# Optimization experiments

Hardware: AMD Instinct MI355X
Metric: run time of the kernel (lower is better)

## Reference

```python
import jax, jax.numpy as jnp
import numpy as np

B, T, D, H = 4, 2048, 1024, 16
HS = D // H  # 64
EPS = 1e-5


def layer_norm(x, g, b):
    mu = jnp.mean(x, axis=-1, keepdims=True)
    var = jnp.mean(jnp.square(x - mu), axis=-1, keepdims=True)
    return (x - mu) * jax.lax.rsqrt(var + EPS) * g + b


def setup_inputs() -> dict:
    key = jax.random.key(0)
    ks = jax.random.split(key, 12)
    s_in = 1.0 / np.sqrt(D)
    s_proj = 1.0 / np.sqrt(H * HS)
    s_ff = 1.0 / np.sqrt(4 * D)
    return {
        "x": jax.random.normal(ks[0], (B, T, D), jnp.float32),
        "ln1_g": jnp.ones((D,), jnp.float32),
        "ln1_b": jnp.zeros((D,), jnp.float32),
        # per-head Q/K/V weights stacked: [H, D, HS] (x @ W, no bias)
        "wq": jax.random.uniform(ks[1], (H, D, HS), jnp.float32, -s_in, s_in),
        "wk": jax.random.uniform(ks[2], (H, D, HS), jnp.float32, -s_in, s_in),
        "wv": jax.random.uniform(ks[3], (H, D, HS), jnp.float32, -s_in, s_in),
        "w_proj": jax.random.uniform(ks[4], (H * HS, D), jnp.float32, -s_proj, s_proj),
        "b_proj": jax.random.uniform(ks[5], (D,), jnp.float32, -s_proj, s_proj),
        "ln2_g": jnp.ones((D,), jnp.float32),
        "ln2_b": jnp.zeros((D,), jnp.float32),
        "w1": jax.random.uniform(ks[6], (D, 4 * D), jnp.float32, -s_in, s_in),
        "b1": jax.random.uniform(ks[7], (4 * D,), jnp.float32, -s_in, s_in),
        "w2": jax.random.uniform(ks[8], (4 * D, D), jnp.float32, -s_ff, s_ff),
        "b2": jax.random.uniform(ks[9], (D,), jnp.float32, -s_ff, s_ff),
    }


def reference(x, ln1_g, ln1_b, wq, wk, wv, w_proj, b_proj, ln2_g, ln2_b, w1, b1, w2, b2):
    # --- pre-LN self-attention ---
    xn = layer_norm(x, ln1_g, ln1_b)
    q = jnp.einsum("btd,hdk->bhtk", xn, wq)
    k = jnp.einsum("btd,hdk->bhtk", xn, wk)
    v = jnp.einsum("btd,hdk->bhtk", xn, wv)
    scale = HS ** -0.5
    scores = jnp.einsum("bhtk,bhsk->bhts", q, k) * scale  # [B,H,T,T]
    t = x.shape[1]
    causal = jnp.tril(jnp.ones((t, t), bool))
    scores = jnp.where(causal, scores, -jnp.inf)
    attn = jax.nn.softmax(scores, axis=-1)  # dropout p=0 -> identity
    ctx = jnp.einsum("bhts,bhsk->bhtk", attn, v)
    ctx = jnp.transpose(ctx, (0, 2, 1, 3)).reshape(x.shape[0], t, H * HS)
    x = x + ctx @ w_proj + b_proj
    # --- pre-LN feed-forward ---
    xn = layer_norm(x, ln2_g, ln2_b)
    h = jax.nn.relu(xn @ w1 + b1)
    return x + h @ w2 + b2
```

## Files before the change

### kernel.cpp

```cpp
#include <hip/hip_runtime.h>

typedef __bf16 bf16;
typedef __attribute__((ext_vector_type(8))) __bf16 bf16x8;
typedef __attribute__((ext_vector_type(4))) __bf16 bf16x4;
typedef __attribute__((ext_vector_type(4))) float f32x4;

static constexpr int Bc = 4, Tc = 2048, Dc = 1024, Hc = 16, HSc = 64, DFF = 4096;
static constexpr int Mrows = Bc * Tc;

#define DEV __device__ __forceinline__

DEV void load_lds16(const void* g, void* l) {
  __builtin_amdgcn_global_load_lds(
      (const __attribute__((address_space(1))) void*)g,
      (__attribute__((address_space(3))) void*)l, 16, 0, 0);
}

__global__ void repack_qkv_kernel(const float* __restrict__ wq,
                                  const float* __restrict__ wk,
                                  const float* __restrict__ wv,
                                  bf16* __restrict__ dst) {
  __shared__ float tile[64][65];
  const int dblk = blockIdx.x;
  const int z = blockIdx.y;
  const int w = z >> 4, h = z & 15;
  const float* src = (w == 0 ? wq : (w == 1 ? wk : wv)) + (size_t)h * Dc * HSc;
  const int tx = threadIdx.x, ty = threadIdx.y;
#pragma unroll
  for (int i = 0; i < 16; ++i)
    tile[ty + i * 4][tx] = src[(size_t)(dblk * 64 + ty + i * 4) * HSc + tx];
  __syncthreads();
#pragma unroll
  for (int i = 0; i < 16; ++i) {
    const int s = ty + i * 4;
    dst[((size_t)w * 1024 + h * 64 + s) * Dc + dblk * 64 + tx] = (bf16)tile[tx][s];
  }
}

__global__ void transpose_to_bf16_kernel(const float* __restrict__ src,
                                         bf16* __restrict__ dst, int R, int C) {
  __shared__ float tile[64][65];
  const int r0 = blockIdx.x * 64, c0 = blockIdx.y * 64;
  const int tx = threadIdx.x, ty = threadIdx.y;
#pragma unroll
  for (int i = 0; i < 16; ++i)
    tile[ty + i * 4][tx] = src[(size_t)(r0 + ty + i * 4) * C + c0 + tx];
  __syncthreads();
#pragma unroll
  for (int i = 0; i < 16; ++i)
    dst[(size_t)(c0 + ty + i * 4) * R + r0 + tx] = (bf16)tile[tx][ty + i * 4];
}

__global__ __launch_bounds__(256) void ln_kernel(const float* __restrict__ x,
                                                 const float* __restrict__ gam,
                                                 const float* __restrict__ bet,
                                                 bf16* __restrict__ out) {
  const int row = blockIdx.x;
  const int t = threadIdx.x;
  const float4 v = ((const float4*)(x + (size_t)row * Dc))[t];
  float s = v.x + v.y + v.z + v.w;
  float s2 = v.x * v.x + v.y * v.y + v.z * v.z + v.w * v.w;
#pragma unroll
  for (int m = 1; m < 64; m <<= 1) {
    s += __shfl_xor(s, m);
    s2 += __shfl_xor(s2, m);
  }
  __shared__ float red[8];
  const int wid = t >> 6;
  if ((t & 63) == 0) { red[wid * 2] = s; red[wid * 2 + 1] = s2; }
  __syncthreads();
  s = red[0] + red[2] + red[4] + red[6];
  s2 = red[1] + red[3] + red[5] + red[7];
  const float mean = s * (1.f / Dc);
  const float var = s2 * (1.f / Dc) - mean * mean;
  const float rstd = rsqrtf(var + 1e-5f);
  const float4 gv = ((const float4*)gam)[t];
  const float4 bv = ((const float4*)bet)[t];
  bf16x4 o;
  o[0] = (bf16)((v.x - mean) * rstd * gv.x + bv.x);
  o[1] = (bf16)((v.y - mean) * rstd * gv.y + bv.y);
  o[2] = (bf16)((v.z - mean) * rstd * gv.z + bv.z);
  o[3] = (bf16)((v.w - mean) * rstd * gv.w + bv.w);
  *(bf16x4*)(out + (size_t)row * Dc + t * 4) = o;
}

template <int MODE, int KTOT, int NSTRIDE>
__global__ __launch_bounds__(256, 2) void gemm_kernel(
    const bf16* __restrict__ A, const bf16* __restrict__ BT,
    const float* __restrict__ bias, const float* __restrict__ resid,
    float* __restrict__ outf, bf16* __restrict__ outb,
    bf16* __restrict__ qo, bf16* __restrict__ ko, bf16* __restrict__ vto) {
  __shared__ __attribute__((aligned(16))) bf16 As[128 * 32];
  __shared__ __attribute__((aligned(16))) bf16 Bs[128 * 32];
  const int tid = threadIdx.x;
  const int wid = tid >> 6, lane = tid & 63;
  const int g = lane >> 4, c = lane & 15;
  const int wr = wid >> 1, wc = wid & 1;
  const int bm = blockIdx.x, bn = blockIdx.y;

  f32x4 acc[4][4];
#pragma unroll
  for (int i = 0; i < 4; ++i)
#pragma unroll
    for (int j = 0; j < 4; ++j)
#pragma unroll
      for (int r = 0; r < 4; ++r) acc[i][j][r] = 0.f;

  const bf16* gA = A + (size_t)(bm * 128 + wid * 32 + (lane >> 2)) * KTOT + (lane & 3) * 8;
  const bf16* gB = BT + (size_t)(bn * 128 + wid * 32 + (lane >> 2)) * KTOT + (lane & 3) * 8;
  bf16* lA0 = &As[(wid * 32) * 32];
  bf16* lA1 = &As[(wid * 32 + 16) * 32];
  bf16* lB0 = &Bs[(wid * 32) * 32];
  bf16* lB1 = &Bs[(wid * 32 + 16) * 32];

  for (int kt = 0; kt < KTOT / 32; ++kt) {
    load_lds16(gA, lA0);
    load_lds16(gA + (size_t)16 * KTOT, lA1);
    load_lds16(gB, lB0);
    load_lds16(gB + (size_t)16 * KTOT, lB1);
    gA += 32;
    gB += 32;
    __syncthreads();
    bf16x8 af[4], bfr[4];
#pragma unroll
    for (int mi = 0; mi < 4; ++mi)
      af[mi] = *(const bf16x8*)&As[(wr * 64 + mi * 16 + c) * 32 + g * 8];
#pragma unroll
    for (int ni = 0; ni < 4; ++ni)
      bfr[ni] = *(const bf16x8*)&Bs[(wc * 64 + ni * 16 + c) * 32 + g * 8];
#pragma unroll
    for (int mi = 0; mi < 4; ++mi)
#pragma unroll
      for (int ni = 0; ni < 4; ++ni)
        acc[mi][ni] =
            __builtin_amdgcn_mfma_f32_16x16x32_bf16(af[mi], bfr[ni], acc[mi][ni], 0, 0, 0);
    __syncthreads();
  }

#pragma unroll
  for (int ni = 0; ni < 4; ++ni) {
    const int n = bn * 128 + wc * 64 + ni * 16 + c;
    float bi = 0.f;
    if (MODE != 0) bi = bias[n];
#pragma unroll
    for (int mi = 0; mi < 4; ++mi) {
      const int m0 = bm * 128 + wr * 64 + mi * 16 + g * 4;
      if (MODE == 0) {
        const int w = n >> 10, n1 = n & 1023, h = n1 >> 6, sidx = n1 & 63;
        const int b = m0 >> 11, t0 = m0 & 2047;
        if (w == 0) {
#pragma unroll
          for (int r = 0; r < 4; ++r)
            qo[(size_t)(b * Hc + h) * (Tc * HSc) + (size_t)(t0 + r) * HSc + sidx] =
                (bf16)(acc[mi][ni][r] * 0.125f);
        } else if (w == 1) {
#pragma unroll
          for (int r = 0; r < 4; ++r)
            ko[(size_t)(b * Hc + h) * (Tc * HSc) + (size_t)(t0 + r) * HSc + sidx] =
                (bf16)acc[mi][ni][r];
        } else {
          bf16x4 pk;
#pragma unroll
          for (int r = 0; r < 4; ++r) pk[r] = (bf16)acc[mi][ni][r];
          *(bf16x4*)&vto[((size_t)(b * Hc + h) * HSc + sidx) * Tc + t0] = pk;
        }
      } else if (MODE == 1 || MODE == 3) {
#pragma unroll
        for (int r = 0; r < 4; ++r) {
          const size_t idx = (size_t)(m0 + r) * NSTRIDE + n;
          outf[idx] = acc[mi][ni][r] + bi + resid[idx];
        }
      } else {
#pragma unroll
        for (int r = 0; r < 4; ++r)
          outb[(size_t)(m0 + r) * NSTRIDE + n] = (bf16)fmaxf(acc[mi][ni][r] + bi, 0.f);
      }
    }
  }
}

__global__ __launch_bounds__(64, 2) void attn_kernel(const bf16* __restrict__ q,
                                                     const bf16* __restrict__ k,
                                                     const bf16* __restrict__ vt,
                                                     bf16* __restrict__ ctx) {
  __shared__ __attribute__((aligned(16))) bf16 P[32][72];
  const int d0 = blockIdx.x;
  const int L = (d0 & 7) * 256 + (d0 >> 3);
  const int bh = L >> 5, w = L & 31;
  const int lane = threadIdx.x;
  const int g = lane >> 4, c = lane & 15;
  const bf16* qh = q + (size_t)bh * Tc * HSc;
  const bf16* kh = k + (size_t)bh * Tc * HSc;
  const bf16* vh = vt + (size_t)bh * HSc * Tc;
  const int b = bh >> 4, h = bh & 15;

  for (int half = 0; half < 2; ++half) {
    const int qt = half ? w : 63 - w;
    const int ktmax = (qt * 32 + 31) >> 6;
    const bf16* qb = qh + (size_t)qt * 32 * HSc;

    bf16x8 qf[2][2];
#pragma unroll
    for (int mi = 0; mi < 2; ++mi)
#pragma unroll
      for (int kk = 0; kk < 2; ++kk)
        qf[mi][kk] = *(const bf16x8*)&qb[(size_t)(mi * 16 + c) * HSc + kk * 32 + g * 8];

    f32x4 o[2][4];
    float m_[2][4], ls[2][4];
#pragma unroll
    for (int mi = 0; mi < 2; ++mi)
#pragma unroll
      for (int r = 0; r < 4; ++r) {
        m_[mi][r] = -1e30f;
        ls[mi][r] = 0.f;
#pragma unroll
        for (int di = 0; di < 4; ++di) o[mi][di][r] = 0.f;
      }

    auto loadK = [&](bf16x8 (&kf)[4][2], int kt) {
      const bf16* kb = kh + (size_t)kt * 64 * HSc;
#pragma unroll
      for (int ni = 0; ni < 4; ++ni)
#pragma unroll
        for (int kk = 0; kk < 2; ++kk)
          kf[ni][kk] = *(const bf16x8*)&kb[(size_t)(ni * 16 + c) * HSc + kk * 32 + g * 8];
    };

    auto body = [&](bf16x8 (&kf)[4][2], int kt) {
      const bf16* vb = vh + kt * 64;
      bf16x8 vf[4][2];
#pragma unroll
      for (int di = 0; di < 4; ++di)
#pragma unroll
        for (int kk = 0; kk < 2; ++kk)
          vf[di][kk] = *(const bf16x8*)&vb[(size_t)(di * 16 + c) * Tc + kk * 32 + g * 8];

      f32x4 s[2][4];
#pragma unroll
      for (int mi = 0; mi < 2; ++mi)
#pragma unroll
        for (int ni = 0; ni < 4; ++ni)
#pragma unroll
          for (int r = 0; r < 4; ++r) s[mi][ni][r] = 0.f;
      __builtin_amdgcn_s_setprio(1);
#pragma unroll
      for (int kk = 0; kk < 2; ++kk)
#pragma unroll
        for (int mi = 0; mi < 2; ++mi)
#pragma unroll
          for (int ni = 0; ni < 4; ++ni)
            s[mi][ni] = __builtin_amdgcn_mfma_f32_16x16x32_bf16(qf[mi][kk], kf[ni][kk],
                                                                s[mi][ni], 0, 0, 0);
      __builtin_amdgcn_s_setprio(0);

      if (kt == ktmax) {
#pragma unroll
        for (int mi = 0; mi < 2; ++mi)
#pragma unroll
          for (int ni = 0; ni < 4; ++ni)
#pragma unroll
            for (int r = 0; r < 4; ++r) {
              const int row = qt * 32 + mi * 16 + g * 4 + r;
              const int col = kt * 64 + ni * 16 + c;
              if (col > row) s[mi][ni][r] = -1e30f;
            }
      }

      float pm[2][4];
      int need = 0;
#pragma unroll
      for (int mi = 0; mi < 2; ++mi)
#pragma unroll
        for (int r = 0; r < 4; ++r) {
          pm[mi][r] = fmaxf(fmaxf(s[mi][0][r], s[mi][1][r]), fmaxf(s[mi][2][r], s[mi][3][r]));
          need |= (pm[mi][r] > m_[mi][r] + 8.f) ? 1 : 0;
        }
      if (__any(need)) {
#pragma unroll
        for (int mi = 0; mi < 2; ++mi)
#pragma unroll
          for (int r = 0; r < 4; ++r) {
            float mx = pm[mi][r];
#pragma unroll
            for (int msk = 1; msk < 16; msk <<= 1) mx = fmaxf(mx, __shfl_xor(mx, msk));
            const float mn = fmaxf(m_[mi][r], mx);
            const float al = __expf(m_[mi][r] - mn);
            m_[mi][r] = mn;
            ls[mi][r] *= al;
#pragma unroll
            for (int di = 0; di < 4; ++di) o[mi][di][r] *= al;
          }
      }
#pragma unroll
      for (int mi = 0; mi < 2; ++mi)
#pragma unroll
        for (int r = 0; r < 4; ++r) {
          float ps = 0.f;
#pragma unroll
          for (int ni = 0; ni < 4; ++ni) {
            const float p = __expf(s[mi][ni][r] - m_[mi][r]);
            ps += p;
            P[mi * 16 + g * 4 + r][ni * 16 + c] = (bf16)p;
          }
          ls[mi][r] += ps;
        }
      asm volatile("s_waitcnt lgkmcnt(0)" ::: "memory");
      __builtin_amdgcn_sched_barrier(0);

      bf16x8 pf[2][2];
#pragma unroll
      for (int mi = 0; mi < 2; ++mi)
#pragma unroll
        for (int kk = 0; kk < 2; ++kk)
          pf[mi][kk] = *(const bf16x8*)&P[mi * 16 + c][kk * 32 + g * 8];
      __builtin_amdgcn_s_setprio(1);
#pragma unroll
      for (int kk = 0; kk < 2; ++kk)
#pragma unroll
        for (int mi = 0; mi < 2; ++mi)
#pragma unroll
          for (int di = 0; di < 4; ++di)
            o[mi][di] = __builtin_amdgcn_mfma_f32_16x16x32_bf16(pf[mi][kk], vf[di][kk],
                                                                o[mi][di], 0, 0, 0);
      __builtin_amdgcn_s_setprio(0);
    };

    bf16x8 kfA[4][2], kfB[4][2];
    loadK(kfA, 0);
    int kt = 0;
    while (true) {
      if (kt < ktmax) loadK(kfB, kt + 1);
      body(kfA, kt);
      if (kt >= ktmax) break;
      ++kt;
      if (kt < ktmax) loadK(kfA, kt + 1);
      body(kfB, kt);
      if (kt >= ktmax) break;
      ++kt;
    }

#pragma unroll
    for (int mi = 0; mi < 2; ++mi)
#pragma unroll
      for (int r = 0; r < 4; ++r) {
        float l = ls[mi][r];
#pragma unroll
        for (int msk = 1; msk < 16; msk <<= 1) l += __shfl_xor(l, msk);
        const float inv = 1.f / l;
        const int t = qt * 32 + mi * 16 + g * 4 + r;
#pragma unroll
        for (int di = 0; di < 4; ++di)
          ctx[((size_t)(b * Tc + t)) * Dc + h * 64 + di * 16 + c] =
              (bf16)(o[mi][di][r] * inv);
      }
  }
}

extern "C" void kernel_launch(void* const* d_in, const int* in_sizes, int n_in,
                              void* d_out, int out_size, void* d_ws, size_t ws_size,
                              hipStream_t stream) {
  (void)in_sizes; (void)n_in; (void)out_size; (void)ws_size;
  const float* x      = (const float*)d_in[0];
  const float* ln1_g  = (const float*)d_in[1];
  const float* ln1_b  = (const float*)d_in[2];
  const float* wq     = (const float*)d_in[3];
  const float* wk     = (const float*)d_in[4];
  const float* wv     = (const float*)d_in[5];
  const float* w_proj = (const float*)d_in[6];
  const float* b_proj = (const float*)d_in[7];
  const float* ln2_g  = (const float*)d_in[8];
  const float* ln2_b  = (const float*)d_in[9];
  const float* w1     = (const float*)d_in[10];
  const float* b1     = (const float*)d_in[11];
  const float* w2     = (const float*)d_in[12];
  const float* b2     = (const float*)d_in[13];
  float* out = (float*)d_out;
  char* ws = (char*)d_ws;

  bf16* qbuf   = (bf16*)(ws + 0);
  bf16* kbuf   = (bf16*)(ws + 16777216);
  bf16* vtbuf  = (bf16*)(ws + 33554432);
  bf16* ctxbuf = (bf16*)(ws + 50331648);
  bf16* wqkvT  = (bf16*)(ws + 67108864);
  bf16* hbuf   = (bf16*)(ws + 0);
  bf16* wprojT = (bf16*)(ws + 73400320);
  bf16* w1T    = (bf16*)(ws + 75497472);
  bf16* w2T    = (bf16*)(ws + 83886080);
  bf16* xn     = (bf16*)(ws + 92274688);
  float* x1buf = (float*)(ws + 109051904);

  repack_qkv_kernel<<<dim3(16, 48), dim3(64, 4), 0, stream>>>(wq, wk, wv, wqkvT);
  transpose_to_bf16_kernel<<<dim3(16, 16), dim3(64, 4), 0, stream>>>(w_proj, wprojT, 1024, 1024);
  transpose_to_bf16_kernel<<<dim3(16, 64), dim3(64, 4), 0, stream>>>(w1, w1T, 1024, 4096);
  transpose_to_bf16_kernel<<<dim3(64, 16), dim3(64, 4), 0, stream>>>(w2, w2T, 4096, 1024);

  ln_kernel<<<Mrows, 256, 0, stream>>>(x, ln1_g, ln1_b, xn);
  gemm_kernel<0, 1024, 0><<<dim3(64, 24), 256, 0, stream>>>(
      xn, wqkvT, nullptr, nullptr, nullptr, nullptr, qbuf, kbuf, vtbuf);
  attn_kernel<<<2048, 64, 0, stream>>>(qbuf, kbuf, vtbuf, ctxbuf);
  gemm_kernel<1, 1024, 1024><<<dim3(64, 8), 256, 0, stream>>>(
      ctxbuf, wprojT, b_proj, x, x1buf, nullptr, nullptr, nullptr, nullptr);
  ln_kernel<<<Mrows, 256, 0, stream>>>(x1buf, ln2_g, ln2_b, xn);
  gemm_kernel<2, 1024, 4096><<<dim3(64, 32), 256, 0, stream>>>(
      xn, w1T, b1, nullptr, nullptr, hbuf, nullptr, nullptr, nullptr);
  gemm_kernel<3, 4096, 1024><<<dim3(64, 8), 256, 0, stream>>>(
      hbuf, w2T, b2, x1buf, out, nullptr, nullptr, nullptr, nullptr);
}
```

Baseline: 457.5 us.

## Share K/V tiles across four waves via double-buffered swizzled LDS in attention

The attention kernel moves from single-wave blocks handling 32 query rows to 256-thread blocks where four waves cover 128 consecutive query rows. K and V tiles are staged once per block into double-buffered LDS using direct global-to-LDS loads with an XOR swizzle, so each wave reads them from LDS instead of loading its own copy from global memory. This is meant to cut redundant K/V global traffic and overlap loading with compute. In exchange it adds block-wide barriers each iteration and load imbalance, since waves with fewer causal tiles sit idle while the block stages tiles up to the last wave's limit.

Measured after the change: 392.2 us. -14.3%, faster.

```diff
diff --git a/kernel.cpp b/kernel.cpp
--- a/kernel.cpp
+++ b/kernel.cpp
@@ -179,25 +179,36 @@
   }
 }
 
-__global__ __launch_bounds__(64, 2) void attn_kernel(const bf16* __restrict__ q,
-                                                     const bf16* __restrict__ k,
-                                                     const bf16* __restrict__ vt,
-                                                     bf16* __restrict__ ctx) {
-  __shared__ __attribute__((aligned(16))) bf16 P[32][72];
+__global__ __launch_bounds__(256, 2) void attn_kernel(const bf16* __restrict__ q,
+                                                      const bf16* __restrict__ k,
+                                                      const bf16* __restrict__ vt,
+                                                      bf16* __restrict__ ctx) {
+  __shared__ __attribute__((aligned(16))) bf16 Kl[2][4096];
+  __shared__ __attribute__((aligned(16))) bf16 Vl[2][4096];
+  __shared__ __attribute__((aligned(16))) bf16 P[4][32][72];
   const int d0 = blockIdx.x;
-  const int L = (d0 & 7) * 256 + (d0 >> 3);
-  const int bh = L >> 5, w = L & 31;
-  const int lane = threadIdx.x;
+  const int L = (d0 & 7) * 64 + (d0 >> 3);
+  const int bh = L >> 3, p = L & 7;
+  const int tid = threadIdx.x;
+  const int wid = tid >> 6, lane = tid & 63;
   const int g = lane >> 4, c = lane & 15;
   const bf16* qh = q + (size_t)bh * Tc * HSc;
-  const bf16* kh = k + (size_t)bh * Tc * HSc;
-  const bf16* vh = vt + (size_t)bh * HSc * Tc;
+  const char* kh = (const char*)(k + (size_t)bh * Tc * HSc);
+  const char* vh = (const char*)(vt + (size_t)bh * HSc * Tc);
   const int b = bh >> 4, h = bh & 15;
 
-  for (int half = 0; half < 2; ++half) {
-    const int qt = half ? w : 63 - w;
-    const int ktmax = (qt * 32 + 31) >> 6;
-    const bf16* qb = qh + (size_t)qt * 32 * HSc;
+  const int sw = ((lane >> 3) & 7) << 4;
+  const int soK = (lane * 16) ^ sw;
+  const int vrow = lane >> 3;
+  const int vcol = ((lane & 7) * 16) ^ sw;
+  const int rsw = (c & 7) << 4;
+
+  for (int g2 = 0; g2 < 2; ++g2) {
+    const int grp = g2 ? p : 15 - p;
+    const int ktB = 2 * grp + 1;
+    const int ktW = 2 * grp + (wid >> 1);
+    const int row0 = grp * 128 + wid * 32;
+    const bf16* qb = qh + (size_t)row0 * HSc;
 
     bf16x8 qf[2][2];
 #pragma unroll
@@ -218,126 +229,132 @@
         for (int di = 0; di < 4; ++di) o[mi][di][r] = 0.f;
       }
 
-    auto loadK = [&](bf16x8 (&kf)[4][2], int kt) {
-      const bf16* kb = kh + (size_t)kt * 64 * HSc;
-#pragma unroll
-      for (int ni = 0; ni < 4; ++ni)
+    auto stage = [&](int buf, int kt) {
+      const char* kb = kh + (size_t)kt * 8192;
+      const char* vb = vh + (size_t)kt * 128;
+#pragma unroll
+      for (int i = 0; i < 4; ++i) {
+        const int idx = wid * 4 + i;
+        if (idx < 8) {
+          load_lds16(kb + idx * 1024 + soK, (char*)&Kl[buf][0] + idx * 1024);
+        } else {
+          const int j = idx - 8;
+          load_lds16(vb + (size_t)(j * 8 + vrow) * (Tc * 2) + vcol,
+                     (char*)&Vl[buf][0] + j * 1024);
+        }
+      }
+    };
+
+    stage(0, 0);
+    __syncthreads();
+    int cur = 0;
+    for (int kt = 0; kt <= ktB; ++kt) {
+      if (kt < ktB) stage(cur ^ 1, kt + 1);
+      if (kt <= ktW) {
+        const char* Kb = (const char*)&Kl[cur][0];
+        bf16x8 kf[4][2];
+#pragma unroll
+        for (int ni = 0; ni < 4; ++ni)
+#pragma unroll
+          for (int kk = 0; kk < 2; ++kk)
+            kf[ni][kk] = *(const bf16x8*)(Kb + (ni * 16 + c) * 128 +
+                                          (((kk << 6) | (g << 4)) ^ rsw));
+        f32x4 s[2][4];
+#pragma unroll
+        for (int mi = 0; mi < 2; ++mi)
+#pragma unroll
+          for (int ni = 0; ni < 4; ++ni)
+#pragma unroll
+            for (int r = 0; r < 4; ++r) s[mi][ni][r] = 0.f;
+        __builtin_amdgcn_s_setprio(1);
 #pragma unroll
         for (int kk = 0; kk < 2; ++kk)
-          kf[ni][kk] = *(const bf16x8*)&kb[(size_t)(ni * 16 + c) * HSc + kk * 32 + g * 8];
-    };
-
-    auto body = [&](bf16x8 (&kf)[4][2], int kt) {
-      const bf16* vb = vh + kt * 64;
-      bf16x8 vf[4][2];
-#pragma unroll
-      for (int di = 0; di < 4; ++di)
-#pragma unroll
-        for (int kk = 0; kk < 2; ++kk)
-          vf[di][kk] = *(const bf16x8*)&vb[(size_t)(di * 16 + c) * Tc + kk * 32 + g * 8];
-
-      f32x4 s[2][4];
-#pragma unroll
-      for (int mi = 0; mi < 2; ++mi)
-#pragma unroll
-        for (int ni = 0; ni < 4; ++ni)
-#pragma unroll
-          for (int r = 0; r < 4; ++r) s[mi][ni][r] = 0.f;
-      __builtin_amdgcn_s_setprio(1);
-#pragma unroll
-      for (int kk = 0; kk < 2; ++kk)
+#pragma unroll
+          for (int mi = 0; mi < 2; ++mi)
+#pragma unroll
+            for (int ni = 0; ni < 4; ++ni)
+              s[mi][ni] = __builtin_amdgcn_mfma_f32_16x16x32_bf16(qf[mi][kk], kf[ni][kk],
+                                                                  s[mi][ni], 0, 0, 0);
+        __builtin_amdgcn_s_setprio(0);
+
+        if (kt == ktW) {
+#pragma unroll
+          for (int mi = 0; mi < 2; ++mi)
+#pragma unroll
+            for (int ni = 0; ni < 4; ++ni)
+#pragma unroll
+              for (int r = 0; r < 4; ++r) {
+                const int row = row0 + mi * 16 + g * 4 + r;
+                const int col = kt * 64 + ni * 16 + c;
+                if (col > row) s[mi][ni][r] = -1e30f;
+              }
+        }
+
+        float pm[2][4];
+        int need = 0;
 #pragma unroll
         for (int mi = 0; mi < 2; ++mi)
 #pragma unroll
-          for (int ni = 0; ni < 4; ++ni)
-            s[mi][ni] = __builtin_amdgcn_mfma_f32_16x16x32_bf16(qf[mi][kk], kf[ni][kk],
-                                                                s[mi][ni], 0, 0, 0);
-      __builtin_amdgcn_s_setprio(0);
-
-      if (kt == ktmax) {
+          for (int r = 0; r < 4; ++r) {
+            pm[mi][r] =
+                fmaxf(fmaxf(s[mi][0][r], s[mi][1][r]), fmaxf(s[mi][2][r], s[mi][3][r]));
+            need |= (pm[mi][r] > m_[mi][r] + 8.f) ? 1 : 0;
+          }
+        if (__any(need)) {
+#pragma unroll
+          for (int mi = 0; mi < 2; ++mi)
+#pragma unroll
+            for (int r = 0; r < 4; ++r) {
+              float mx = pm[mi][r];
+#pragma unroll
+              for (int msk = 1; msk < 16; msk <<= 1) mx = fmaxf(mx, __shfl_xor(mx, msk));
+              const float mn = fmaxf(m_[mi][r], mx);
+              const float al = __expf(m_[mi][r] - mn);
+              m_[mi][r] = mn;
+              ls[mi][r] *= al;
+#pragma unroll
+              for (int di = 0; di < 4; ++di) o[mi][di][r] *= al;
+            }
+        }
 #pragma unroll
         for (int mi = 0; mi < 2; ++mi)
 #pragma unroll
-          for (int ni = 0; ni < 4; ++ni)
-#pragma unroll
-            for (int r = 0; r < 4; ++r) {
-              const int row = qt * 32 + mi * 16 + g * 4 + r;
-              const int col = kt * 64 + ni * 16 + c;
-              if (col > row) s[mi][ni][r] = -1e30f;
+          for (int r = 0; r < 4; ++r) {
+            float ps = 0.f;
+#pragma unroll
+            for (int ni = 0; ni < 4; ++ni) {
+              const float pv = __expf(s[mi][ni][r] - m_[mi][r]);
+              ps += pv;
+              P[wid][mi * 16 + g * 4 + r][ni * 16 + c] = (bf16)pv;
             }
+            ls[mi][r] += ps;
+          }
+        asm volatile("s_waitcnt lgkmcnt(0)" ::: "memory");
+        __builtin_amdgcn_sched_barrier(0);
+
+        bf16x8 pf[2][2];
+#pragma unroll
+        for (int mi = 0; mi < 2; ++mi)
+#pragma unroll
+          for (int kk = 0; kk < 2; ++kk)
+            pf[mi][kk] = *(const bf16x8*)&P[wid][mi * 16 + c][kk * 32 + g * 8];
+        const char* Vb = (const char*)&Vl[cur][0];
+#pragma unroll
+        for (int di = 0; di < 4; ++di) {
+          bf16x8 vf0 = *(const bf16x8*)(Vb + (di * 16 + c) * 128 + ((g << 4) ^ rsw));
+          bf16x8 vf1 =
+              *(const bf16x8*)(Vb + (di * 16 + c) * 128 + (((1 << 6) | (g << 4)) ^ rsw));
+          __builtin_amdgcn_s_setprio(1);
+#pragma unroll
+          for (int mi = 0; mi < 2; ++mi) {
+            o[mi][di] = __builtin_amdgcn_mfma_f32_16x16x32_bf16(pf[mi][0], vf0, o[mi][di], 0, 0, 0);
+            o[mi][di] = __builtin_amdgcn_mfma_f32_16x16x32_bf16(pf[mi][1], vf1, o[mi][di], 0, 0, 0);
+          }
+          __builtin_amdgcn_s_setprio(0);
+        }
       }
-
-      float pm[2][4];
-      int need = 0;
-#pragma unroll
-      for (int mi = 0; mi < 2; ++mi)
-#pragma unroll
-        for (int r = 0; r < 4; ++r) {
-          pm[mi][r] = fmaxf(fmaxf(s[mi][0][r], s[mi][1][r]), fmaxf(s[mi][2][r], s[mi][3][r]));
-          need |= (pm[mi][r] > m_[mi][r] + 8.f) ? 1 : 0;
-        }
-      if (__any(need)) {
-#pragma unroll
-        for (int mi = 0; mi < 2; ++mi)
-#pragma unroll
-          for (int r = 0; r < 4; ++r) {
-            float mx = pm[mi][r];
-#pragma unroll
-            for (int msk = 1; msk < 16; msk <<= 1) mx = fmaxf(mx, __shfl_xor(mx, msk));
-            const float mn = fmaxf(m_[mi][r], mx);
-            const float al = __expf(m_[mi][r] - mn);
-            m_[mi][r] = mn;
-            ls[mi][r] *= al;
-#pragma unroll
-            for (int di = 0; di < 4; ++di) o[mi][di][r] *= al;
-          }
-      }
-#pragma unroll
-      for (int mi = 0; mi < 2; ++mi)
-#pragma unroll
-        for (int r = 0; r < 4; ++r) {
-          float ps = 0.f;
-#pragma unroll
-          for (int ni = 0; ni < 4; ++ni) {
-            const float p = __expf(s[mi][ni][r] - m_[mi][r]);
-            ps += p;
-            P[mi * 16 + g * 4 + r][ni * 16 + c] = (bf16)p;
-          }
-          ls[mi][r] += ps;
-        }
-      asm volatile("s_waitcnt lgkmcnt(0)" ::: "memory");
-      __builtin_amdgcn_sched_barrier(0);
-
-      bf16x8 pf[2][2];
-#pragma unroll
-      for (int mi = 0; mi < 2; ++mi)
-#pragma unroll
-        for (int kk = 0; kk < 2; ++kk)
-          pf[mi][kk] = *(const bf16x8*)&P[mi * 16 + c][kk * 32 + g * 8];
-      __builtin_amdgcn_s_setprio(1);
-#pragma unroll
-      for (int kk = 0; kk < 2; ++kk)
-#pragma unroll
-        for (int mi = 0; mi < 2; ++mi)
-#pragma unroll
-          for (int di = 0; di < 4; ++di)
-            o[mi][di] = __builtin_amdgcn_mfma_f32_16x16x32_bf16(pf[mi][kk], vf[di][kk],
-                                                                o[mi][di], 0, 0, 0);
-      __builtin_amdgcn_s_setprio(0);
-    };
-
-    bf16x8 kfA[4][2], kfB[4][2];
-    loadK(kfA, 0);
-    int kt = 0;
-    while (true) {
-      if (kt < ktmax) loadK(kfB, kt + 1);
-      body(kfA, kt);
-      if (kt >= ktmax) break;
-      ++kt;
-      if (kt < ktmax) loadK(kfA, kt + 1);
-      body(kfB, kt);
-      if (kt >= ktmax) break;
-      ++kt;
+      __syncthreads();
+      cur ^= 1;
     }
 
 #pragma unroll
@@ -348,7 +365,7 @@
 #pragma unroll
         for (int msk = 1; msk < 16; msk <<= 1) l += __shfl_xor(l, msk);
         const float inv = 1.f / l;
-        const int t = qt * 32 + mi * 16 + g * 4 + r;
+        const int t = row0 + mi * 16 + g * 4 + r;
 #pragma unroll
         for (int di = 0; di < 4; ++di)
           ctx[((size_t)(b * Tc + t)) * Dc + h * 64 + di * 16 + c] =
@@ -398,7 +415,7 @@
   ln_kernel<<<Mrows, 256, 0, stream>>>(x, ln1_g, ln1_b, xn);
   gemm_kernel<0, 1024, 0><<<dim3(64, 24), 256, 0, stream>>>(
       xn, wqkvT, nullptr, nullptr, nullptr, nullptr, qbuf, kbuf, vtbuf);
-  attn_kernel<<<2048, 64, 0, stream>>>(qbuf, kbuf, vtbuf, ctxbuf);
+  attn_kernel<<<512, 256, 0, stream>>>(qbuf, kbuf, vtbuf, ctxbuf);
   gemm_kernel<1, 1024, 1024><<<dim3(64, 8), 256, 0, stream>>>(
       ctxbuf, wprojT, b_proj, x, x1buf, nullptr, nullptr, nullptr, nullptr);
   ln_kernel<<<Mrows, 256, 0, stream>>>(x1buf, ln2_g, ln2_b, xn);
```
